# Performance work log

Hardware: AMD Instinct MI355X
Metric: run time of the kernel (lower is better)

The kernel has to match this reference:

```python
import jax, jax.numpy as jnp
import numpy as np

TOPK = 2
GATE_THRESHOLD = 0.5
GATE_ALPHA = 0.1
EPS = 1e-8


def setup_inputs() -> dict:
    key = jax.random.key(0)
    x = jax.random.normal(key, (8192, 1024), dtype=jnp.float32)
    return {"x": x}


def reference(x):
    B, D = x.shape
    # F.normalize(p=2, eps): x / max(||x||, eps)
    norm = jnp.linalg.norm(x, axis=-1, keepdims=True)
    xn = x / jnp.maximum(norm, EPS)

    # pairwise dots; diagonal (self) masked to -1; NN search is no_grad
    dots = jax.lax.stop_gradient(xn @ xn.T)  # [B, B]
    diag = jnp.arange(B)
    dots = dots.at[diag, diag].set(-1.0)
    _, idx = jax.lax.top_k(dots, TOPK)  # [B, TOPK]

    nn_vecs = xn[idx]  # [B, TOPK, D]
    # torch PairwiseDistance(2, eps): ||x1 - x2 + eps||_2
    diff = xn[:, None, :] - nn_vecs + EPS
    distances = jnp.sqrt(jnp.sum(diff * diff, axis=-1)).reshape(-1)  # [B*TOPK]
    losses = -jnp.log(distances + EPS)

    # gate enabled since gate_threshold > 0
    alpha = max(GATE_ALPHA, 1e-6)
    gate = jax.nn.sigmoid((losses - GATE_THRESHOLD) / alpha)
    lg = losses * gate
    weighted_mean = lg.mean()
    gated_mean = lg.sum() / jnp.maximum(gate.sum(), 1.0)
    return 0.5 * weighted_mean + 0.5 * gated_mean
```

## Files before the change

### kernel.cpp

```cpp
#include <hip/hip_runtime.h>
#include <math.h>

#define NROWS 8192
#define DIM   1024
#define BT    256
#define NCHUNK 32
#define NTRI  528
#define GRID  512
#define NKT   32
#define BK    32

typedef __bf16 bf16x8 __attribute__((ext_vector_type(8)));
typedef float  f32x4  __attribute__((ext_vector_type(4)));

__device__ __forceinline__ unsigned short f2bf(float f) {
    unsigned int u = __float_as_uint(f);
    u = (u + 0x7FFFu + ((u >> 16) & 1u)) >> 16;
    return (unsigned short)u;
}

__device__ __forceinline__ void gld16(const void* g, void* l) {
    __builtin_amdgcn_global_load_lds(
        (__attribute__((address_space(1))) void*)g,
        (__attribute__((address_space(3))) void*)l,
        16, 0, 0);
}

template<int N>
__device__ __forceinline__ float dppror(float v) {
    return __int_as_float(__builtin_amdgcn_update_dpp(
        0, __float_as_int(v), 0x120 + N, 0xF, 0xF, false));
}

__device__ __forceinline__ void t2push(float& a1, float& a2, float v) {
    float hi = fmaxf(a1, v);
    float lo = fminf(a1, v);
    a1 = hi;
    a2 = fmaxf(a2, lo);
}

__device__ __forceinline__ void t2merge(float& a1, float& a2, float b1, float b2) {
    float hi = fmaxf(a1, b1);
    float lo = fminf(a1, b1);
    a1 = hi;
    a2 = fmaxf(fmaxf(a2, b2), lo);
}

__global__ __launch_bounds__(256) void knorm(const float* __restrict__ x,
                                             unsigned short* __restrict__ xn) {
    const int w = threadIdx.x >> 6, lane = threadIdx.x & 63;
    const int row = blockIdx.x * 4 + w;
    const float4* src = (const float4*)(x + (size_t)row * DIM);
    float4 v[4];
    float ss = 0.0f;
    #pragma unroll
    for (int i = 0; i < 4; i++) {
        v[i] = src[lane + 64 * i];
        ss += v[i].x * v[i].x + v[i].y * v[i].y + v[i].z * v[i].z + v[i].w * v[i].w;
    }
    #pragma unroll
    for (int d = 1; d < 64; d <<= 1) ss += __shfl_xor(ss, d);
    const float inv = 1.0f / fmaxf(sqrtf(ss), 1e-8f);
    unsigned short* dst = xn + (size_t)row * DIM;
    #pragma unroll
    for (int i = 0; i < 4; i++) {
        uint2 o;
        o.x = (unsigned)f2bf(v[i].x * inv) | ((unsigned)f2bf(v[i].y * inv) << 16);
        o.y = (unsigned)f2bf(v[i].z * inv) | ((unsigned)f2bf(v[i].w * inv) << 16);
        *(uint2*)(dst + (size_t)(lane + 64 * i) * 4) = o;
    }
}

__global__ __launch_bounds__(512) void kgram(const unsigned short* __restrict__ xn,
                                             float2* __restrict__ top2) {
    __shared__ __align__(16) char smem[110592];
    float (*st2r)[256][2] = (float (*)[256][2])(smem + 98304);
    float (*st2c)[256][2] = (float (*)[256][2])(smem + 98304 + 8192);

    const int t = threadIdx.x;
    const int lane = t & 63;
    const int w = t >> 6;
    const int wr = w >> 2, wc = w & 3;
    const int g = lane >> 4, c = lane & 15;

    const int LA = c * 64 + (((g ^ (c & 3) ^ ((c >> 2) & 3)) & 3) << 4);

    const int q0 = t, q1 = 512 + t;
    const int r0 = q0 >> 2, g0 = (q0 & 3) ^ (r0 & 3) ^ ((r0 >> 2) & 3);
    const int r1 = q1 >> 2, g1 = (q1 & 3) ^ (r1 & 3) ^ ((r1 >> 2) & 3);

    const int bswz = (blockIdx.x & 7) * (GRID / 8) + (blockIdx.x >> 3);

    for (int tix = bswz; tix < NTRI; tix += GRID) {
        int by = (int)((sqrtf(8.0f * (float)tix + 1.0f) - 1.0f) * 0.5f);
        while ((by + 1) * (by + 2) / 2 <= tix) by++;
        while (by * (by + 1) / 2 > tix) by--;
        const int bx = tix - by * (by + 1) / 2;
        const bool diagTile = (bx == by);

        const unsigned short* sA0 = xn + (size_t)(by * BT + r0) * DIM + g0 * 8;
        const unsigned short* sA1 = xn + (size_t)(by * BT + r1) * DIM + g1 * 8;
        const unsigned short* sB0 = xn + (size_t)(bx * BT + r0) * DIM + g0 * 8;
        const unsigned short* sB1 = xn + (size_t)(bx * BT + r1) * DIM + g1 * 8;

        f32x4 acc[8][4];
        #pragma unroll
        for (int m = 0; m < 8; m++)
            #pragma unroll
            for (int n = 0; n < 4; n++) acc[m][n] = (f32x4)0.0f;

        auto STAGE = [&](int b, int kt) {
            char* base = smem + b * 32768;
            gld16(sA0 + kt * BK, base + q0 * 16);
            gld16(sA1 + kt * BK, base + q1 * 16);
            gld16(sB0 + kt * BK, base + 16384 + q0 * 16);
            gld16(sB1 + kt * BK, base + 16384 + q1 * 16);
        };

        STAGE(0, 0);
        STAGE(1, 1);
        asm volatile("s_waitcnt vmcnt(4)" ::: "memory");
        __builtin_amdgcn_s_barrier();
        asm volatile("" ::: "memory");
        __builtin_amdgcn_sched_barrier(0);

        int cur = 0;
        #pragma unroll 1
        for (int kt = 0; kt < NKT; ++kt) {
            if (kt + 2 < NKT) {
                int nb = cur + 2; if (nb >= 3) nb -= 3;
                STAGE(nb, kt + 2);
            }
            const char* Ab = smem + cur * 32768 + wr * 8192 + LA;
            const char* Bb = smem + cur * 32768 + 16384 + wc * 4096 + LA;
            bf16x8 b0 = *(const bf16x8*)(Bb + 0 * 1024);
            bf16x8 b1 = *(const bf16x8*)(Bb + 1 * 1024);
            bf16x8 b2 = *(const bf16x8*)(Bb + 2 * 1024);
            bf16x8 b3 = *(const bf16x8*)(Bb + 3 * 1024);
            #pragma unroll
            for (int ph = 0; ph < 2; ++ph) {
                bf16x8 a0 = *(const bf16x8*)(Ab + (ph * 4 + 0) * 1024);
                bf16x8 a1 = *(const bf16x8*)(Ab + (ph * 4 + 1) * 1024);
                bf16x8 a2 = *(const bf16x8*)(Ab + (ph * 4 + 2) * 1024);
                bf16x8 a3 = *(const bf16x8*)(Ab + (ph * 4 + 3) * 1024);
                asm volatile("s_waitcnt lgkmcnt(0)" ::: "memory");
                __builtin_amdgcn_sched_barrier(0);
                __builtin_amdgcn_s_setprio(1);
                acc[ph*4+0][0] = __builtin_amdgcn_mfma_f32_16x16x32_bf16(a0, b0, acc[ph*4+0][0], 0, 0, 0);
                acc[ph*4+0][1] = __builtin_amdgcn_mfma_f32_16x16x32_bf16(a0, b1, acc[ph*4+0][1], 0, 0, 0);
                acc[ph*4+0][2] = __builtin_amdgcn_mfma_f32_16x16x32_bf16(a0, b2, acc[ph*4+0][2], 0, 0, 0);
                acc[ph*4+0][3] = __builtin_amdgcn_mfma_f32_16x16x32_bf16(a0, b3, acc[ph*4+0][3], 0, 0, 0);
                acc[ph*4+1][0] = __builtin_amdgcn_mfma_f32_16x16x32_bf16(a1, b0, acc[ph*4+1][0], 0, 0, 0);
                acc[ph*4+1][1] = __builtin_amdgcn_mfma_f32_16x16x32_bf16(a1, b1, acc[ph*4+1][1], 0, 0, 0);
                acc[ph*4+1][2] = __builtin_amdgcn_mfma_f32_16x16x32_bf16(a1, b2, acc[ph*4+1][2], 0, 0, 0);
                acc[ph*4+1][3] = __builtin_amdgcn_mfma_f32_16x16x32_bf16(a1, b3, acc[ph*4+1][3], 0, 0, 0);
                acc[ph*4+2][0] = __builtin_amdgcn_mfma_f32_16x16x32_bf16(a2, b0, acc[ph*4+2][0], 0, 0, 0);
                acc[ph*4+2][1] = __builtin_amdgcn_mfma_f32_16x16x32_bf16(a2, b1, acc[ph*4+2][1], 0, 0, 0);
                acc[ph*4+2][2] = __builtin_amdgcn_mfma_f32_16x16x32_bf16(a2, b2, acc[ph*4+2][2], 0, 0, 0);
                acc[ph*4+2][3] = __builtin_amdgcn_mfma_f32_16x16x32_bf16(a2, b3, acc[ph*4+2][3], 0, 0, 0);
                acc[ph*4+3][0] = __builtin_amdgcn_mfma_f32_16x16x32_bf16(a3, b0, acc[ph*4+3][0], 0, 0, 0);
                acc[ph*4+3][1] = __builtin_amdgcn_mfma_f32_16x16x32_bf16(a3, b1, acc[ph*4+3][1], 0, 0, 0);
                acc[ph*4+3][2] = __builtin_amdgcn_mfma_f32_16x16x32_bf16(a3, b2, acc[ph*4+3][2], 0, 0, 0);
                acc[ph*4+3][3] = __builtin_amdgcn_mfma_f32_16x16x32_bf16(a3, b3, acc[ph*4+3][3], 0, 0, 0);
                __builtin_amdgcn_s_setprio(0);
                __builtin_amdgcn_sched_barrier(0);
            }
            if (kt + 1 < NKT) {
                if (kt + 2 < NKT) asm volatile("s_waitcnt vmcnt(4)" ::: "memory");
                else              asm volatile("s_waitcnt vmcnt(0)" ::: "memory");
                __builtin_amdgcn_s_barrier();
                asm volatile("" ::: "memory");
                __builtin_amdgcn_sched_barrier(0);
            }
            cur = cur + 1; if (cur >= 3) cur -= 3;
        }

        #pragma unroll
        for (int m = 0; m < 8; m++) {
            #pragma unroll
            for (int rr = 0; rr < 4; rr++) {
                const int lrow = wr * 128 + m * 16 + g * 4 + rr;
                float a1 = -1e30f, a2 = -1e30f;
                #pragma unroll
                for (int n = 0; n < 4; n++) {
                    float v = acc[m][n][rr];
                    if (diagTile && (wc * 64 + n * 16 + c) == lrow) v = -2.0f;
                    t2push(a1, a2, v);
                }
                { float b1 = dppror<1>(a1), b2 = dppror<1>(a2); t2merge(a1, a2, b1, b2); }
                { float b1 = dppror<2>(a1), b2 = dppror<2>(a2); t2merge(a1, a2, b1, b2); }
                { float b1 = dppror<4>(a1), b2 = dppror<4>(a2); t2merge(a1, a2, b1, b2); }
                { float b1 = dppror<8>(a1), b2 = dppror<8>(a2); t2merge(a1, a2, b1, b2); }
                if (c == 0) { st2r[wc][lrow][0] = a1; st2r[wc][lrow][1] = a2; }
            }
        }
        if (!diagTile) {
            #pragma unroll
            for (int n = 0; n < 4; n++) {
                const int lcol = wc * 64 + n * 16 + c;
                float a1 = -1e30f, a2 = -1e30f;
                #pragma unroll
                for (int m = 0; m < 8; m++)
                    #pragma unroll
                    for (int rr = 0; rr < 4; rr++)
                        t2push(a1, a2, acc[m][n][rr]);
                #pragma unroll
                for (int d = 16; d < 64; d <<= 1) {
                    float b1 = __shfl_xor(a1, d);
                    float b2 = __shfl_xor(a2, d);
                    t2merge(a1, a2, b1, b2);
                }
                if (g == 0) { st2c[wr][lcol][0] = a1; st2c[wr][lcol][1] = a2; }
            }
        }
        __syncthreads();
        if (t < 256) {
            float a1 = st2r[0][t][0], a2 = st2r[0][t][1];
            t2merge(a1, a2, st2r[1][t][0], st2r[1][t][1]);
            t2merge(a1, a2, st2r[2][t][0], st2r[2][t][1]);
            t2merge(a1, a2, st2r[3][t][0], st2r[3][t][1]);
            top2[(size_t)(by * BT + t) * NCHUNK + bx] = make_float2(a1, a2);
        } else if (!diagTile) {
            const int tc = t - 256;
            float a1 = st2c[0][tc][0], a2 = st2c[0][tc][1];
            t2merge(a1, a2, st2c[1][tc][0], st2c[1][tc][1]);
            top2[(size_t)(bx * BT + tc) * NCHUNK + by] = make_float2(a1, a2);
        }
        __syncthreads();
    }
}

__global__ __launch_bounds__(256) void kloss(const float2* __restrict__ top2,
                                             float2* __restrict__ partials) {
    const int t = threadIdx.x;
    const int w = t >> 6, lane = t & 63;
    const int row = blockIdx.x * 4 + w;
    float a1 = -1e30f, a2 = -1e30f;
    if (lane < NCHUNK) {
        float2 q = top2[(size_t)row * NCHUNK + lane];
        a1 = q.x; a2 = q.y;
    }
    #pragma unroll
    for (int d = 1; d < 64; d <<= 1) {
        float b1 = __shfl_xor(a1, d);
        float b2 = __shfl_xor(a2, d);
        t2merge(a1, a2, b1, b2);
    }
    __shared__ float2 wsum[4];
    if (lane == 0) {
        float slg = 0.0f, sg = 0.0f;
        float vs[2] = {a1, a2};
        #pragma unroll
        for (int i = 0; i < 2; i++) {
            float dd = sqrtf(fmaxf(2.0f - 2.0f * vs[i], 0.0f));
            float loss = -logf(dd + 1e-8f);
            float gate = 1.0f / (1.0f + expf(-(loss - 0.5f) * 10.0f));
            slg += loss * gate;
            sg += gate;
        }
        wsum[w] = make_float2(slg, sg);
    }
    __syncthreads();
    if (t == 0) {
        float a = 0.0f, b = 0.0f;
        #pragma unroll
        for (int i = 0; i < 4; i++) { a += wsum[i].x; b += wsum[i].y; }
        partials[blockIdx.x] = make_float2(a, b);
    }
}

__global__ __launch_bounds__(256) void kfinal(const float2* __restrict__ partials,
                                              float* __restrict__ out) {
    const int t = threadIdx.x;
    float a = 0.0f, b = 0.0f;
    for (int i = t; i < 2048; i += 256) {
        float2 p = partials[i];
        a += p.x; b += p.y;
    }
    #pragma unroll
    for (int d = 1; d < 64; d <<= 1) {
        a += __shfl_xor(a, d);
        b += __shfl_xor(b, d);
    }
    __shared__ float2 ws4[4];
    if ((t & 63) == 0) ws4[t >> 6] = make_float2(a, b);
    __syncthreads();
    if (t == 0) {
        float A = 0.0f, Bb = 0.0f;
        #pragma unroll
        for (int i = 0; i < 4; i++) { A += ws4[i].x; Bb += ws4[i].y; }
        float wm = A / 16384.0f;
        float gm = A / fmaxf(Bb, 1.0f);
        out[0] = 0.5f * wm + 0.5f * gm;
    }
}

extern "C" void kernel_launch(void* const* d_in, const int* in_sizes, int n_in,
                              void* d_out, int out_size, void* d_ws, size_t ws_size,
                              hipStream_t stream) {
    const float* x = (const float*)d_in[0];
    unsigned short* xn = (unsigned short*)d_ws;
    float2* top2 = (float2*)((char*)d_ws + (size_t)16 * 1024 * 1024);
    float2* partials = (float2*)((char*)d_ws + (size_t)20 * 1024 * 1024);
    float* out = (float*)d_out;

    knorm<<<NROWS / 4, 256, 0, stream>>>(x, xn);
    kgram<<<GRID, 512, 0, stream>>>(xn, top2);
    kloss<<<2048, 256, 0, stream>>>(top2, partials);
    kfinal<<<1, 256, 0, stream>>>(partials, out);
}
```

Before: 184.0 us.

## Deepen Gram-kernel pipeline to 4 LDS stages with register double-buffered fragments

Moves the bf16 Gram GEMM main loop from a 3-buffer LDS ring to a 4-buffer ring with three tiles prefetched ahead. A/B MFMA fragments are now double-buffered in registers, so the LDS reads for step k+1 are issued while the MFMAs for step k run. The LDS XOR swizzle is changed and launch_bounds gains a waves-per-EU hint. Shared memory grows to 140 KB and register pressure rises from the extra fragment sets, which risks spills or lower occupancy.

```diff
diff --git a/kernel.cpp b/kernel.cpp
--- a/kernel.cpp
+++ b/kernel.cpp
@@ -71,11 +71,11 @@
     }
 }
 
-__global__ __launch_bounds__(512) void kgram(const unsigned short* __restrict__ xn,
-                                             float2* __restrict__ top2) {
-    __shared__ __align__(16) char smem[110592];
-    float (*st2r)[256][2] = (float (*)[256][2])(smem + 98304);
-    float (*st2c)[256][2] = (float (*)[256][2])(smem + 98304 + 8192);
+__global__ __launch_bounds__(512, 2) void kgram(const unsigned short* __restrict__ xn,
+                                                float2* __restrict__ top2) {
+    __shared__ __align__(16) char smem[143360];
+    float (*st2r)[256][2] = (float (*)[256][2])(smem + 131072);
+    float (*st2c)[256][2] = (float (*)[256][2])(smem + 131072 + 8192);
 
     const int t = threadIdx.x;
     const int lane = t & 63;
@@ -83,11 +83,11 @@
     const int wr = w >> 2, wc = w & 3;
     const int g = lane >> 4, c = lane & 15;
 
-    const int LA = c * 64 + (((g ^ (c & 3) ^ ((c >> 2) & 3)) & 3) << 4);
+    const int LA = c * 64 + (((g ^ ((c >> 1) & 3)) & 3) << 4);
 
     const int q0 = t, q1 = 512 + t;
-    const int r0 = q0 >> 2, g0 = (q0 & 3) ^ (r0 & 3) ^ ((r0 >> 2) & 3);
-    const int r1 = q1 >> 2, g1 = (q1 & 3) ^ (r1 & 3) ^ ((r1 >> 2) & 3);
+    const int r0 = q0 >> 2, g0 = (q0 & 3) ^ ((r0 >> 1) & 3);
+    const int r1 = q1 >> 2, g1 = (q1 & 3) ^ ((r1 >> 1) & 3);
 
     const int bswz = (blockIdx.x & 7) * (GRID / 8) + (blockIdx.x >> 3);
 
@@ -109,71 +109,86 @@
             #pragma unroll
             for (int n = 0; n < 4; n++) acc[m][n] = (f32x4)0.0f;
 
-        auto STAGE = [&](int b, int kt) {
-            char* base = smem + b * 32768;
-            gld16(sA0 + kt * BK, base + q0 * 16);
-            gld16(sA1 + kt * BK, base + q1 * 16);
-            gld16(sB0 + kt * BK, base + 16384 + q0 * 16);
-            gld16(sB1 + kt * BK, base + 16384 + q1 * 16);
-        };
+        bf16x8 afA[8], bfA[4], afB[8], bfB[4];
+
+#define STAGE(BUF, KT) do {                                  \
+        char* _b = smem + (BUF) * 32768;                     \
+        gld16(sA0 + (KT) * BK, _b + q0 * 16);                \
+        gld16(sA1 + (KT) * BK, _b + q1 * 16);                \
+        gld16(sB0 + (KT) * BK, _b + 16384 + q0 * 16);        \
+        gld16(sB1 + (KT) * BK, _b + 16384 + q1 * 16);        \
+    } while (0)
+
+#define LDFRAG(AF, BF, BUF) do {                                          \
+        const char* _ab = smem + (BUF) * 32768 + wr * 8192 + LA;          \
+        const char* _bb = smem + (BUF) * 32768 + 16384 + wc * 4096 + LA;  \
+        AF[0] = *(const bf16x8*)(_ab + 0 * 1024);                         \
+        AF[1] = *(const bf16x8*)(_ab + 1 * 1024);                         \
+        AF[2] = *(const bf16x8*)(_ab + 2 * 1024);                         \
+        AF[3] = *(const bf16x8*)(_ab + 3 * 1024);                         \
+        AF[4] = *(const bf16x8*)(_ab + 4 * 1024);                         \
+        AF[5] = *(const bf16x8*)(_ab + 5 * 1024);                         \
+        AF[6] = *(const bf16x8*)(_ab + 6 * 1024);                         \
+        AF[7] = *(const bf16x8*)(_ab + 7 * 1024);                         \
+        BF[0] = *(const bf16x8*)(_bb + 0 * 1024);                         \
+        BF[1] = *(const bf16x8*)(_bb + 1 * 1024);                         \
+        BF[2] = *(const bf16x8*)(_bb + 2 * 1024);                         \
+        BF[3] = *(const bf16x8*)(_bb + 3 * 1024);                         \
+    } while (0)
+
+#define MFMA32(AF, BF) do {                                               \
+        _Pragma("unroll")                                                 \
+        for (int _m = 0; _m < 8; _m++)                                    \
+            _Pragma("unroll")                                             \
+            for (int _n = 0; _n < 4; _n++)                                \
+                acc[_m][_n] = __builtin_amdgcn_mfma_f32_16x16x32_bf16(    \
+                    AF[_m], BF[_n], acc[_m][_n], 0, 0, 0);                \
+    } while (0)
+
+#define KBODY(KT_STAGE, DO_STAGE, VM, LGK, CURA, CURB, NXTA, NXTB, NBUF)  \
+    do {                                                                  \
+        asm volatile("s_waitcnt vmcnt(" #VM ")" ::: "memory");            \
+        __builtin_amdgcn_s_barrier();                                     \
+        __builtin_amdgcn_sched_barrier(0);                                \
+        LDFRAG(NXTA, NXTB, (NBUF));                                       \
+        if (DO_STAGE) STAGE(((NBUF) + 2) & 3, (KT_STAGE));                \
+        asm volatile("s_waitcnt lgkmcnt(" #LGK ")" ::: "memory");         \
+        __builtin_amdgcn_sched_barrier(0);                                \
+        __builtin_amdgcn_s_setprio(1);                                    \
+        MFMA32(CURA, CURB);                                               \
+        __builtin_amdgcn_s_setprio(0);                                    \
+        __builtin_amdgcn_sched_barrier(0);                                \
+    } while (0)
 
         STAGE(0, 0);
         STAGE(1, 1);
-        asm volatile("s_waitcnt vmcnt(4)" ::: "memory");
+        STAGE(2, 2);
+        asm volatile("s_waitcnt vmcnt(8)" ::: "memory");
         __builtin_amdgcn_s_barrier();
-        asm volatile("" ::: "memory");
         __builtin_amdgcn_sched_barrier(0);
-
-        int cur = 0;
-        #pragma unroll 1
-        for (int kt = 0; kt < NKT; ++kt) {
-            if (kt + 2 < NKT) {
-                int nb = cur + 2; if (nb >= 3) nb -= 3;
-                STAGE(nb, kt + 2);
-            }
-            const char* Ab = smem + cur * 32768 + wr * 8192 + LA;
-            const char* Bb = smem + cur * 32768 + 16384 + wc * 4096 + LA;
-            bf16x8 b0 = *(const bf16x8*)(Bb + 0 * 1024);
-            bf16x8 b1 = *(const bf16x8*)(Bb + 1 * 1024);
-            bf16x8 b2 = *(const bf16x8*)(Bb + 2 * 1024);
-            bf16x8 b3 = *(const bf16x8*)(Bb + 3 * 1024);
-            #pragma unroll
-            for (int ph = 0; ph < 2; ++ph) {
-                bf16x8 a0 = *(const bf16x8*)(Ab + (ph * 4 + 0) * 1024);
-                bf16x8 a1 = *(const bf16x8*)(Ab + (ph * 4 + 1) * 1024);
-                bf16x8 a2 = *(const bf16x8*)(Ab + (ph * 4 + 2) * 1024);
-                bf16x8 a3 = *(const bf16x8*)(Ab + (ph * 4 + 3) * 1024);
-                asm volatile("s_waitcnt lgkmcnt(0)" ::: "memory");
-                __builtin_amdgcn_sched_barrier(0);
-                __builtin_amdgcn_s_setprio(1);
-                acc[ph*4+0][0] = __builtin_amdgcn_mfma_f32_16x16x32_bf16(a0, b0, acc[ph*4+0][0], 0, 0, 0);
-                acc[ph*4+0][1] = __builtin_amdgcn_mfma_f32_16x16x32_bf16(a0, b1, acc[ph*4+0][1], 0, 0, 0);
-                acc[ph*4+0][2] = __builtin_amdgcn_mfma_f32_16x16x32_bf16(a0, b2, acc[ph*4+0][2], 0, 0, 0);
-                acc[ph*4+0][3] = __builtin_amdgcn_mfma_f32_16x16x32_bf16(a0, b3, acc[ph*4+0][3], 0, 0, 0);
-                acc[ph*4+1][0] = __builtin_amdgcn_mfma_f32_16x16x32_bf16(a1, b0, acc[ph*4+1][0], 0, 0, 0);
-                acc[ph*4+1][1] = __builtin_amdgcn_mfma_f32_16x16x32_bf16(a1, b1, acc[ph*4+1][1], 0, 0, 0);
-                acc[ph*4+1][2] = __builtin_amdgcn_mfma_f32_16x16x32_bf16(a1, b2, acc[ph*4+1][2], 0, 0, 0);
-                acc[ph*4+1][3] = __builtin_amdgcn_mfma_f32_16x16x32_bf16(a1, b3, acc[ph*4+1][3], 0, 0, 0);
-                acc[ph*4+2][0] = __builtin_amdgcn_mfma_f32_16x16x32_bf16(a2, b0, acc[ph*4+2][0], 0, 0, 0);
-                acc[ph*4+2][1] = __builtin_amdgcn_mfma_f32_16x16x32_bf16(a2, b1, acc[ph*4+2][1], 0, 0, 0);
-                acc[ph*4+2][2] = __builtin_amdgcn_mfma_f32_16x16x32_bf16(a2, b2, acc[ph*4+2][2], 0, 0, 0);
-                acc[ph*4+2][3] = __builtin_amdgcn_mfma_f32_16x16x32_bf16(a2, b3, acc[ph*4+2][3], 0, 0, 0);
-                acc[ph*4+3][0] = __builtin_amdgcn_mfma_f32_16x16x32_bf16(a3, b0, acc[ph*4+3][0], 0, 0, 0);
-                acc[ph*4+3][1] = __builtin_amdgcn_mfma_f32_16x16x32_bf16(a3, b1, acc[ph*4+3][1], 0, 0, 0);
-                acc[ph*4+3][2] = __builtin_amdgcn_mfma_f32_16x16x32_bf16(a3, b2, acc[ph*4+3][2], 0, 0, 0);
-                acc[ph*4+3][3] = __builtin_amdgcn_mfma_f32_16x16x32_bf16(a3, b3, acc[ph*4+3][3], 0, 0, 0);
-                __builtin_amdgcn_s_setprio(0);
-                __builtin_amdgcn_sched_barrier(0);
-            }
-            if (kt + 1 < NKT) {
-                if (kt + 2 < NKT) asm volatile("s_waitcnt vmcnt(4)" ::: "memory");
-                else              asm volatile("s_waitcnt vmcnt(0)" ::: "memory");
-                __builtin_amdgcn_s_barrier();
-                asm volatile("" ::: "memory");
-                __builtin_amdgcn_sched_barrier(0);
-            }
-            cur = cur + 1; if (cur >= 3) cur -= 3;
-        }
+        LDFRAG(afA, bfA, 0);
+
+        for (int jj = 0; jj < 7; ++jj) {
+            const int j0 = 4 * jj;
+            KBODY(j0 + 3, 1, 4, 12, afA, bfA, afB, bfB, 1);
+            KBODY(j0 + 4, 1, 4, 12, afB, bfB, afA, bfA, 2);
+            KBODY(j0 + 5, 1, 4, 12, afA, bfA, afB, bfB, 3);
+            KBODY(j0 + 6, 1, 4, 12, afB, bfB, afA, bfA, 0);
+        }
+        KBODY(31, 1, 4, 12, afA, bfA, afB, bfB, 1);
+        KBODY(0,  0, 4, 12, afB, bfB, afA, bfA, 2);
+        KBODY(0,  0, 0, 12, afA, bfA, afB, bfB, 3);
+        asm volatile("s_waitcnt lgkmcnt(0)" ::: "memory");
+        __builtin_amdgcn_sched_barrier(0);
+        __builtin_amdgcn_s_setprio(1);
+        MFMA32(afB, bfB);
+        __builtin_amdgcn_s_setprio(0);
+        __builtin_amdgcn_sched_barrier(0);
+
+#undef KBODY
+#undef MFMA32
+#undef LDFRAG
+#undef STAGE
 
         #pragma unroll
         for (int m = 0; m < 8; m++) {
```

After: 233.5 us. 26.9% more time.
